# Kernel optimization log

Measured on AMD Instinct MI355X. Metric: run time of the kernel, lower is better.

Reference implementation:

```python
import jax, jax.numpy as jnp
import numpy as np

BLOCK = 8
SCALE = 0.5  # deterministic choice from scale_factors=[0.5, 0.75]


def setup_inputs() -> dict:
    key = jax.random.key(0)
    k1, k2 = jax.random.split(key)
    B, C, H, W = 32, 3, 512, 512
    x = jax.random.uniform(k1, (B, C, H, W), dtype=jnp.float32) * 2.0 - 1.0  # images in [-1,1]
    # per-8x8-block uniform values u in [0,1); noise = (u - 0.5)/50
    block_noise = jax.random.uniform(k2, (B, H // BLOCK, W // BLOCK), dtype=jnp.float32)
    return {"x": x, "block_noise": block_noise}


def reference(x, block_noise):
    B, C, H, W = x.shape
    nH, nW = int(H * SCALE), int(W * SCALE)
    # bilinear down then up, half-pixel centers == torch align_corners=False
    x_ds = jax.image.resize(x, (B, C, nH, nW), method="bilinear")
    x_rec = jax.image.resize(x_ds, (B, C, H, W), method="bilinear")
    # block noise: one scalar per 8x8 block, broadcast over channels
    noise = (block_noise - 0.5) / 50.0  # [B, H/8, W/8]
    noise_full = jnp.repeat(jnp.repeat(noise, BLOCK, axis=1), BLOCK, axis=2)  # [B, H, W]
    out = jnp.clip(x_rec + noise_full[:, None, :, :], -1.0, 1.0)
    return out
```

## Files before the change

kernel.cpp:

```cpp
#include <hip/hip_runtime.h>


typedef float f32x4 __attribute__((ext_vector_type(4)));

namespace {
constexpr int IMG = 512;
constexpr int TY = 16;
constexpr int HROWS = TY + 6;
constexpr float I32 = 1.0f / 32.0f;
constexpr float I7  = 1.0f / 7.0f;
constexpr float I28 = 1.0f / 28.0f;
}

__device__ __forceinline__ f32x4 vfma(float w, f32x4 a, f32x4 acc) {
  acc.x = fmaf(w, a.x, acc.x); acc.y = fmaf(w, a.y, acc.y);
  acc.z = fmaf(w, a.z, acc.z); acc.w = fmaf(w, a.w, acc.w);
  return acc;
}
__device__ __forceinline__ f32x4 vmul(float w, f32x4 a) {
  f32x4 r; r.x = w * a.x; r.y = w * a.y; r.z = w * a.z; r.w = w * a.w;
  return r;
}

__global__ __launch_bounds__(512) void compress_fused5_kernel(
    const float* __restrict__ x, const float* __restrict__ bn,
    float* __restrict__ out) {
  const int nwg = gridDim.x;
  const int cpx = nwg >> 3;
  const int bid = blockIdx.x;
  const int logical = (bid & 7) * cpx + (bid >> 3);
  const int ty = logical & 31;
  const int plane = logical >> 5;
  const int b = plane / 3;
  const int y0 = ty * TY;
  const int tid = threadIdx.x;
  const int cg = tid & 127;
  const int ts = tid >> 7;
  const int gx0 = 4 * cg;

  __shared__ float H[HROWS][IMG];
  __shared__ float nz[128];

  const float* xp = x + (size_t)plane * (IMG * IMG);
  float* op = out + (size_t)plane * (IMG * IMG);

  if (tid < 128) {
    const int brow = (y0 >> 3) + (tid >> 6);
    const int bcol = tid & 63;
    nz[tid] = (bn[(size_t)b * 4096 + brow * 64 + bcol] - 0.5f) * 0.02f;
  }

  const bool left  = (cg == 0);
  const bool right = (cg == 127);
  const int A0 = left ? 0 : (right ? IMG - 12 : gx0 - 4);

  auto rowptr = [&](int r) -> const f32x4* {
    int g = y0 - 3 + r;
    g = max(0, min(IMG - 1, g));
    return (const f32x4*)(xp + (size_t)g * IMG + A0);
  };

  f32x4 qa, qb, qc;
  { const f32x4* p = rowptr(ts); qa = p[0]; qb = p[1]; qc = p[2]; }

#pragma unroll
  for (int k = 0; k < 6; ++k) {
    const int r = ts + 4 * k;
    const int rn = r + 4;
    f32x4 na, nb, nc;
    if (rn < HROWS) { const f32x4* p = rowptr(rn); na = p[0]; nb = p[1]; nc = p[2]; }
    if (r < HROWS) {
      const float f0 = qa.x, f1 = qa.y, f2 = qa.z, f3 = qa.w;
      const float f4_ = qb.x, f5 = qb.y, f6 = qb.z, f7 = qb.w;
      const float f8 = qc.x, f9 = qc.y, f10 = qc.z, f11 = qc.w;
      f32x4 h;
      if (left) {
        h.x = (3.f * f0 + 3.f * f1 + f2) * I7;
        h.y = 9*I28*f0 + (9*I28 + I32)*f1 + (3*I28 + 3*I32)*f2 + 3*I32*f3 + I32*f4_;
        h.z = 3*I28*f0 + (3*I28 + 3*I32)*f1 + (I28 + 9*I32)*f2 + 9*I32*f3 + 3*I32*f4_;
        h.w = (3.f*f1 + 9.f*f2 + 10.f*f3 + 6.f*f4_ + 3.f*f5 + f6) * I32;
      } else if (right) {
        h.x = (f5 + 3.f*f6 + 6.f*f7 + 10.f*f8 + 9.f*f9 + 3.f*f10) * I32;
        h.y = 3*I32*f7 + 9*I32*f8 + (I28 + 9*I32)*f9 + (3*I28 + 3*I32)*f10 + 3*I28*f11;
        h.z = I32*f7 + 3*I32*f8 + (3*I28 + 3*I32)*f9 + (9*I28 + I32)*f10 + 9*I28*f11;
        h.w = (f9 + 3.f*f10 + 3.f*f11) * I7;
      } else {
        h.x = (f1 + 3.f*f2 + 6.f*f3 + 10.f*f4_ + 9.f*f5 + 3.f*f6) * I32;
        h.y = (3.f*f3 + 9.f*f4_ + 10.f*f5 + 6.f*f6 + 3.f*f7 + f8) * I32;
        h.z = (f3 + 3.f*f4_ + 6.f*f5 + 10.f*f6 + 9.f*f7 + 3.f*f8) * I32;
        h.w = (3.f*f5 + 9.f*f6 + 10.f*f7 + 6.f*f8 + 3.f*f9 + f10) * I32;
      }
      *(f32x4*)&H[r][gx0] = h;
    }
    if (rn < HROWS) { qa = na; qb = nb; qc = nc; }
  }
  __syncthreads();

  const int wb = 4 * ts;
  const float nzv = nz[((ts >> 1) << 6) + (cg >> 1)];
  const bool top = (y0 == 0 && ts == 0);
  const bool bot = (y0 == IMG - TY && ts == 3);
  const int gy0 = y0 + 4 * ts;

#define LDQ(j) (*(const f32x4*)&H[wb + (j)][gx0])
#define FINISH_STORE(o, ii)                                                    \
  {                                                                            \
    f32x4 v = o;                                                               \
    v.x = fminf(1.f, fmaxf(-1.f, v.x + nzv));                                  \
    v.y = fminf(1.f, fmaxf(-1.f, v.y + nzv));                                  \
    v.z = fminf(1.f, fmaxf(-1.f, v.z + nzv));                                  \
    v.w = fminf(1.f, fmaxf(-1.f, v.w + nzv));                                  \
    __builtin_nontemporal_store(v, (f32x4*)(op + (size_t)(gy0 + ii) * IMG + gx0)); \
  }

  const f32x4 q0 = LDQ(0), q1 = LDQ(1), q2 = LDQ(2);
  const f32x4 q3 = LDQ(3), q4 = LDQ(4), q5 = LDQ(5);

  f32x4 o0;
  if (top) {
    o0 = vfma(3*I7, q3, vfma(3*I7, q4, vmul(I7, q5)));
  } else {
    o0 = vfma(I32, q0, vfma(3*I32, q1, vfma(6*I32, q2,
         vfma(10*I32, q3, vfma(9*I32, q4, vmul(3*I32, q5))))));
  }
  FINISH_STORE(o0, 0)

  const f32x4 q6 = LDQ(6), q7 = LDQ(7);
  f32x4 o1, o2;
  if (top) {
    o1 = vfma(9*I28, q3, vfma(9*I28 + I32, q4,
         vfma(3*I28 + 3*I32, q5, vfma(3*I32, q6, vmul(I32, q7)))));
    o2 = vfma(3*I28, q3, vfma(3*I28 + 3*I32, q4,
         vfma(I28 + 9*I32, q5, vfma(9*I32, q6, vmul(3*I32, q7)))));
  } else if (bot) {
    o1 = vfma(3*I32, q2, vfma(9*I32, q3, vfma(I28 + 9*I32, q4,
         vfma(3*I28 + 3*I32, q5, vmul(3*I28, q6)))));
    o2 = vfma(I32, q2, vfma(3*I32, q3, vfma(3*I28 + 3*I32, q4,
         vfma(9*I28 + I32, q5, vmul(9*I28, q6)))));
  } else {
    o1 = vfma(3*I32, q2, vfma(9*I32, q3, vfma(10*I32, q4,
         vfma(6*I32, q5, vfma(3*I32, q6, vmul(I32, q7))))));
    o2 = vfma(I32, q2, vfma(3*I32, q3, vfma(6*I32, q4,
         vfma(10*I32, q5, vfma(9*I32, q6, vmul(3*I32, q7))))));
  }
  FINISH_STORE(o1, 1)
  FINISH_STORE(o2, 2)

  const f32x4 q8 = LDQ(8), q9 = LDQ(9);
  f32x4 o3;
  if (bot) {
    o3 = vfma(I7, q4, vfma(3*I7, q5, vmul(3*I7, q6)));
  } else {
    o3 = vfma(3*I32, q4, vfma(9*I32, q5, vfma(10*I32, q6,
         vfma(6*I32, q7, vfma(3*I32, q8, vmul(I32, q9))))));
  }
  FINISH_STORE(o3, 3)
#undef FINISH_STORE
#undef LDQ
}

extern "C" void kernel_launch(void* const* d_in, const int* in_sizes, int n_in,
                              void* d_out, int out_size, void* d_ws, size_t ws_size,
                              hipStream_t stream) {
  const float* x  = (const float*)d_in[0];
  const float* bn = (const float*)d_in[1];
  float* out = (float*)d_out;

  const int n_planes = in_sizes[0] / (IMG * IMG);
  const int nwg = (IMG / TY) * n_planes;
  compress_fused5_kernel<<<dim3(nwg), dim3(512), 0, stream>>>(x, bn, out);
}
```

Before: 35.97 us.

## Make workgroups persistent over several row tiles with register prefetch of next tile

```diff
diff --git a/kernel.cpp b/kernel.cpp
--- a/kernel.cpp
+++ b/kernel.cpp
@@ -7,6 +7,7 @@
 constexpr int IMG = 512;
 constexpr int TY = 16;
 constexpr int HROWS = TY + 6;
+constexpr int TPB = 6;
 constexpr float I32 = 1.0f / 32.0f;
 constexpr float I7  = 1.0f / 7.0f;
 constexpr float I28 = 1.0f / 28.0f;
@@ -22,141 +23,150 @@
   return r;
 }
 
-__global__ __launch_bounds__(512) void compress_fused5_kernel(
+__global__ __launch_bounds__(512, 4) void compress_fused11_kernel(
     const float* __restrict__ x, const float* __restrict__ bn,
     float* __restrict__ out) {
-  const int nwg = gridDim.x;
-  const int cpx = nwg >> 3;
   const int bid = blockIdx.x;
-  const int logical = (bid & 7) * cpx + (bid >> 3);
-  const int ty = logical & 31;
-  const int plane = logical >> 5;
-  const int b = plane / 3;
-  const int y0 = ty * TY;
+  const int cpx = gridDim.x >> 3;
+  const int sw = (bid & 7) * cpx + (bid >> 3);
+  const int base = sw * TPB;
   const int tid = threadIdx.x;
   const int cg = tid & 127;
   const int ts = tid >> 7;
   const int gx0 = 4 * cg;
 
   __shared__ float H[HROWS][IMG];
-  __shared__ float nz[128];
-
-  const float* xp = x + (size_t)plane * (IMG * IMG);
-  float* op = out + (size_t)plane * (IMG * IMG);
-
-  if (tid < 128) {
-    const int brow = (y0 >> 3) + (tid >> 6);
-    const int bcol = tid & 63;
-    nz[tid] = (bn[(size_t)b * 4096 + brow * 64 + bcol] - 0.5f) * 0.02f;
-  }
 
   const bool left  = (cg == 0);
   const bool right = (cg == 127);
   const int A0 = left ? 0 : (right ? IMG - 12 : gx0 - 4);
 
-  auto rowptr = [&](int r) -> const f32x4* {
-    int g = y0 - 3 + r;
-    g = max(0, min(IMG - 1, g));
-    return (const f32x4*)(xp + (size_t)g * IMG + A0);
+  auto hconv = [&](f32x4 qa, f32x4 qb, f32x4 qc) -> f32x4 {
+    const float f0 = qa.x, f1 = qa.y, f2 = qa.z, f3 = qa.w;
+    const float f4_ = qb.x, f5 = qb.y, f6 = qb.z, f7 = qb.w;
+    const float f8 = qc.x, f9 = qc.y, f10 = qc.z, f11 = qc.w;
+    f32x4 h;
+    if (left) {
+      h.x = (3.f * f0 + 3.f * f1 + f2) * I7;
+      h.y = 9*I28*f0 + (9*I28 + I32)*f1 + (3*I28 + 3*I32)*f2 + 3*I32*f3 + I32*f4_;
+      h.z = 3*I28*f0 + (3*I28 + 3*I32)*f1 + (I28 + 9*I32)*f2 + 9*I32*f3 + 3*I32*f4_;
+      h.w = (3.f*f1 + 9.f*f2 + 10.f*f3 + 6.f*f4_ + 3.f*f5 + f6) * I32;
+    } else if (right) {
+      h.x = (f5 + 3.f*f6 + 6.f*f7 + 10.f*f8 + 9.f*f9 + 3.f*f10) * I32;
+      h.y = 3*I32*f7 + 9*I32*f8 + (I28 + 9*I32)*f9 + (3*I28 + 3*I32)*f10 + 3*I28*f11;
+      h.z = I32*f7 + 3*I32*f8 + (3*I28 + 3*I32)*f9 + (9*I28 + I32)*f10 + 9*I28*f11;
+      h.w = (f9 + 3.f*f10 + 3.f*f11) * I7;
+    } else {
+      h.x = (f1 + 3.f*f2 + 6.f*f3 + 10.f*f4_ + 9.f*f5 + 3.f*f6) * I32;
+      h.y = (3.f*f3 + 9.f*f4_ + 10.f*f5 + 6.f*f6 + 3.f*f7 + f8) * I32;
+      h.z = (f3 + 3.f*f4_ + 6.f*f5 + 10.f*f6 + 9.f*f7 + 3.f*f8) * I32;
+      h.w = (3.f*f5 + 9.f*f6 + 10.f*f7 + 6.f*f8 + 3.f*f9 + f10) * I32;
+    }
+    return h;
   };
 
-  f32x4 qa, qb, qc;
-  { const f32x4* p = rowptr(ts); qa = p[0]; qb = p[1]; qc = p[2]; }
+  f32x4 A[6], B[6], C[6];
+
+  auto prefetch = [&](int logical) {
+    const int plane = logical >> 5;
+    const int y0 = (logical & 31) * TY;
+    const float* xp = x + (size_t)plane * (IMG * IMG);
+#pragma unroll
+    for (int k = 0; k < 6; ++k) {
+      const int r = ts + 4 * k;
+      if (r < HROWS) {
+        int g = y0 - 3 + r;
+        g = max(0, min(IMG - 1, g));
+        const f32x4* p = (const f32x4*)(xp + (size_t)g * IMG + A0);
+        A[k] = p[0]; B[k] = p[1]; C[k] = p[2];
+      }
+    }
+  };
+
+  prefetch(base);
+
+  for (int i = 0; i < TPB; ++i) {
+    const int logical = base + i;
+    const int plane = logical >> 5;
+    const int ty = logical & 31;
+    const int y0 = ty * TY;
+    const int b = plane / 3;
+    float* op = out + (size_t)plane * (IMG * IMG);
+
+    __syncthreads();
 
 #pragma unroll
-  for (int k = 0; k < 6; ++k) {
-    const int r = ts + 4 * k;
-    const int rn = r + 4;
-    f32x4 na, nb, nc;
-    if (rn < HROWS) { const f32x4* p = rowptr(rn); na = p[0]; nb = p[1]; nc = p[2]; }
-    if (r < HROWS) {
-      const float f0 = qa.x, f1 = qa.y, f2 = qa.z, f3 = qa.w;
-      const float f4_ = qb.x, f5 = qb.y, f6 = qb.z, f7 = qb.w;
-      const float f8 = qc.x, f9 = qc.y, f10 = qc.z, f11 = qc.w;
-      f32x4 h;
-      if (left) {
-        h.x = (3.f * f0 + 3.f * f1 + f2) * I7;
-        h.y = 9*I28*f0 + (9*I28 + I32)*f1 + (3*I28 + 3*I32)*f2 + 3*I32*f3 + I32*f4_;
-        h.z = 3*I28*f0 + (3*I28 + 3*I32)*f1 + (I28 + 9*I32)*f2 + 9*I32*f3 + 3*I32*f4_;
-        h.w = (3.f*f1 + 9.f*f2 + 10.f*f3 + 6.f*f4_ + 3.f*f5 + f6) * I32;
-      } else if (right) {
-        h.x = (f5 + 3.f*f6 + 6.f*f7 + 10.f*f8 + 9.f*f9 + 3.f*f10) * I32;
-        h.y = 3*I32*f7 + 9*I32*f8 + (I28 + 9*I32)*f9 + (3*I28 + 3*I32)*f10 + 3*I28*f11;
-        h.z = I32*f7 + 3*I32*f8 + (3*I28 + 3*I32)*f9 + (9*I28 + I32)*f10 + 9*I28*f11;
-        h.w = (f9 + 3.f*f10 + 3.f*f11) * I7;
-      } else {
-        h.x = (f1 + 3.f*f2 + 6.f*f3 + 10.f*f4_ + 9.f*f5 + 3.f*f6) * I32;
-        h.y = (3.f*f3 + 9.f*f4_ + 10.f*f5 + 6.f*f6 + 3.f*f7 + f8) * I32;
-        h.z = (f3 + 3.f*f4_ + 6.f*f5 + 10.f*f6 + 9.f*f7 + 3.f*f8) * I32;
-        h.w = (3.f*f5 + 9.f*f6 + 10.f*f7 + 6.f*f8 + 3.f*f9 + f10) * I32;
-      }
-      *(f32x4*)&H[r][gx0] = h;
+    for (int k = 0; k < 6; ++k) {
+      const int r = ts + 4 * k;
+      if (r < HROWS) *(f32x4*)&H[r][gx0] = hconv(A[k], B[k], C[k]);
     }
-    if (rn < HROWS) { qa = na; qb = nb; qc = nc; }
-  }
-  __syncthreads();
+    __syncthreads();
 
-  const int wb = 4 * ts;
-  const float nzv = nz[((ts >> 1) << 6) + (cg >> 1)];
-  const bool top = (y0 == 0 && ts == 0);
-  const bool bot = (y0 == IMG - TY && ts == 3);
-  const int gy0 = y0 + 4 * ts;
+    if (i + 1 < TPB) prefetch(logical + 1);
+
+    const int wb = 4 * ts;
+    const float nzv =
+        (bn[(size_t)b * 4096 + ((y0 >> 3) + (ts >> 1)) * 64 + (cg >> 1)] - 0.5f) * 0.02f;
+    const bool top = (y0 == 0 && ts == 0);
+    const bool bot = (y0 == IMG - TY && ts == 3);
+    const int gy0 = y0 + 4 * ts;
 
 #define LDQ(j) (*(const f32x4*)&H[wb + (j)][gx0])
 #define FINISH_STORE(o, ii)                                                    \
-  {                                                                            \
-    f32x4 v = o;                                                               \
-    v.x = fminf(1.f, fmaxf(-1.f, v.x + nzv));                                  \
-    v.y = fminf(1.f, fmaxf(-1.f, v.y + nzv));                                  \
-    v.z = fminf(1.f, fmaxf(-1.f, v.z + nzv));                                  \
-    v.w = fminf(1.f, fmaxf(-1.f, v.w + nzv));                                  \
-    __builtin_nontemporal_store(v, (f32x4*)(op + (size_t)(gy0 + ii) * IMG + gx0)); \
-  }
+    {                                                                          \
+      f32x4 v = o;                                                             \
+      v.x = fminf(1.f, fmaxf(-1.f, v.x + nzv));                                \
+      v.y = fminf(1.f, fmaxf(-1.f, v.y + nzv));                                \
+      v.z = fminf(1.f, fmaxf(-1.f, v.z + nzv));                                \
+      v.w = fminf(1.f, fmaxf(-1.f, v.w + nzv));                                \
+      __builtin_nontemporal_store(v, (f32x4*)(op + (size_t)(gy0 + ii) * IMG + gx0)); \
+    }
 
-  const f32x4 q0 = LDQ(0), q1 = LDQ(1), q2 = LDQ(2);
-  const f32x4 q3 = LDQ(3), q4 = LDQ(4), q5 = LDQ(5);
+    const f32x4 q0 = LDQ(0), q1 = LDQ(1), q2 = LDQ(2);
+    const f32x4 q3 = LDQ(3), q4 = LDQ(4), q5 = LDQ(5);
 
-  f32x4 o0;
-  if (top) {
-    o0 = vfma(3*I7, q3, vfma(3*I7, q4, vmul(I7, q5)));
-  } else {
-    o0 = vfma(I32, q0, vfma(3*I32, q1, vfma(6*I32, q2,
-         vfma(10*I32, q3, vfma(9*I32, q4, vmul(3*I32, q5))))));
-  }
-  FINISH_STORE(o0, 0)
+    f32x4 o0;
+    if (top) {
+      o0 = vfma(3*I7, q3, vfma(3*I7, q4, vmul(I7, q5)));
+    } else {
+      o0 = vfma(I32, q0, vfma(3*I32, q1, vfma(6*I32, q2,
+           vfma(10*I32, q3, vfma(9*I32, q4, vmul(3*I32, q5))))));
+    }
+    FINISH_STORE(o0, 0)
 
-  const f32x4 q6 = LDQ(6), q7 = LDQ(7);
-  f32x4 o1, o2;
-  if (top) {
-    o1 = vfma(9*I28, q3, vfma(9*I28 + I32, q4,
-         vfma(3*I28 + 3*I32, q5, vfma(3*I32, q6, vmul(I32, q7)))));
-    o2 = vfma(3*I28, q3, vfma(3*I28 + 3*I32, q4,
-         vfma(I28 + 9*I32, q5, vfma(9*I32, q6, vmul(3*I32, q7)))));
-  } else if (bot) {
-    o1 = vfma(3*I32, q2, vfma(9*I32, q3, vfma(I28 + 9*I32, q4,
-         vfma(3*I28 + 3*I32, q5, vmul(3*I28, q6)))));
-    o2 = vfma(I32, q2, vfma(3*I32, q3, vfma(3*I28 + 3*I32, q4,
-         vfma(9*I28 + I32, q5, vmul(9*I28, q6)))));
-  } else {
-    o1 = vfma(3*I32, q2, vfma(9*I32, q3, vfma(10*I32, q4,
-         vfma(6*I32, q5, vfma(3*I32, q6, vmul(I32, q7))))));
-    o2 = vfma(I32, q2, vfma(3*I32, q3, vfma(6*I32, q4,
-         vfma(10*I32, q5, vfma(9*I32, q6, vmul(3*I32, q7))))));
-  }
-  FINISH_STORE(o1, 1)
-  FINISH_STORE(o2, 2)
+    const f32x4 q6 = LDQ(6), q7 = LDQ(7);
+    f32x4 o1, o2;
+    if (top) {
+      o1 = vfma(9*I28, q3, vfma(9*I28 + I32, q4,
+           vfma(3*I28 + 3*I32, q5, vfma(3*I32, q6, vmul(I32, q7)))));
+      o2 = vfma(3*I28, q3, vfma(3*I28 + 3*I32, q4,
+           vfma(I28 + 9*I32, q5, vfma(9*I32, q6, vmul(3*I32, q7)))));
+    } else if (bot) {
+      o1 = vfma(3*I32, q2, vfma(9*I32, q3, vfma(I28 + 9*I32, q4,
+           vfma(3*I28 + 3*I32, q5, vmul(3*I28, q6)))));
+      o2 = vfma(I32, q2, vfma(3*I32, q3, vfma(3*I28 + 3*I32, q4,
+           vfma(9*I28 + I32, q5, vmul(9*I28, q6)))));
+    } else {
+      o1 = vfma(3*I32, q2, vfma(9*I32, q3, vfma(10*I32, q4,
+           vfma(6*I32, q5, vfma(3*I32, q6, vmul(I32, q7))))));
+      o2 = vfma(I32, q2, vfma(3*I32, q3, vfma(6*I32, q4,
+           vfma(10*I32, q5, vfma(9*I32, q6, vmul(3*I32, q7))))));
+    }
+    FINISH_STORE(o1, 1)
+    FINISH_STORE(o2, 2)
 
-  const f32x4 q8 = LDQ(8), q9 = LDQ(9);
-  f32x4 o3;
-  if (bot) {
-    o3 = vfma(I7, q4, vfma(3*I7, q5, vmul(3*I7, q6)));
-  } else {
-    o3 = vfma(3*I32, q4, vfma(9*I32, q5, vfma(10*I32, q6,
-         vfma(6*I32, q7, vfma(3*I32, q8, vmul(I32, q9))))));
-  }
-  FINISH_STORE(o3, 3)
+    const f32x4 q8 = LDQ(8), q9 = LDQ(9);
+    f32x4 o3;
+    if (bot) {
+      o3 = vfma(I7, q4, vfma(3*I7, q5, vmul(3*I7, q6)));
+    } else {
+      o3 = vfma(3*I32, q4, vfma(9*I32, q5, vfma(10*I32, q6,
+           vfma(6*I32, q7, vfma(3*I32, q8, vmul(I32, q9))))));
+    }
+    FINISH_STORE(o3, 3)
 #undef FINISH_STORE
 #undef LDQ
+  }
 }
 
 extern "C" void kernel_launch(void* const* d_in, const int* in_sizes, int n_in,
@@ -167,6 +177,7 @@
   float* out = (float*)d_out;
 
   const int n_planes = in_sizes[0] / (IMG * IMG);
-  const int nwg = (IMG / TY) * n_planes;
-  compress_fused5_kernel<<<dim3(nwg), dim3(512), 0, stream>>>(x, bn, out);
+  const int n_tiles = (IMG / TY) * n_planes;
+  const int nwg = n_tiles / TPB;
+  compress_fused11_kernel<<<dim3(nwg), dim3(512), 0, stream>>>(x, bn, out);
 }
```

New measurement: 40.71 us. 13.2% more time.
